# Kernel optimization log

Hardware: AMD Instinct MI355X
Metric: run time of the kernel (lower is better)

The kernel has to match this reference:

```python
import jax, jax.numpy as jnp
import numpy as np

N = 50000
E = 800000
F_IN = 256
HEADS = 4
C = 64
NEG_SLOPE = 0.2


def setup_inputs() -> dict:
    key = jax.random.key(0)
    ks = jax.random.split(key, 7)
    x = jax.random.normal(ks[0], (N, F_IN), dtype=jnp.float32)
    edge_index = jax.random.randint(ks[1], (2, E), 0, N, dtype=jnp.int64)
    # Glorot-ish scaling for weights
    W = jax.random.normal(ks[2], (F_IN, HEADS * C), dtype=jnp.float32) / np.sqrt(F_IN)
    att_src = jax.random.normal(ks[3], (HEADS, C), dtype=jnp.float32) / np.sqrt(C)
    att_dst = jax.random.normal(ks[4], (HEADS, C), dtype=jnp.float32) / np.sqrt(C)
    bias = jnp.zeros((HEADS * C,), dtype=jnp.float32)
    prelu_a = jnp.full((1,), 0.25, dtype=jnp.float32)  # PReLU default init
    return {"x": x, "edge_index": edge_index, "W": W, "att_src": att_src,
            "att_dst": att_dst, "bias": bias, "prelu_a": prelu_a}


def _gat_forward(x, edge_index, W, att_src, att_dst, bias, prelu_a):
    n = x.shape[0]
    # add self loops (PyG GATConv default)
    loops = jnp.arange(n, dtype=edge_index.dtype)
    src = jnp.concatenate([edge_index[0], loops])  # message source j
    dst = jnp.concatenate([edge_index[1], loops])  # message target i

    h = (x @ W).reshape(n, HEADS, C)                    # [N,H,C]
    a_src = jnp.einsum('nhc,hc->nh', h, att_src)        # [N,H]
    a_dst = jnp.einsum('nhc,hc->nh', h, att_dst)        # [N,H]

    e = a_src[src] + a_dst[dst]                         # [Etot,H]
    e = jnp.where(e >= 0, e, NEG_SLOPE * e)             # LeakyReLU(0.2)

    # numerically stable softmax over edges grouped by destination node
    m = jax.ops.segment_max(e, dst, num_segments=n)     # [N,H]
    alpha = jnp.exp(e - m[dst])
    denom = jax.ops.segment_sum(alpha, dst, num_segments=n)
    alpha = alpha / (denom[dst] + 1e-16)                # [Etot,H]

    msg = alpha[:, :, None] * h[src]                    # [Etot,H,C]
    out = jax.ops.segment_sum(msg, dst, num_segments=n) # [N,H,C]
    out = out.reshape(n, HEADS * C) + bias
    # PReLU with single shared parameter
    return jnp.where(out >= 0, out, prelu_a * out)


def reference(x, edge_index, W, att_src, att_dst, bias, prelu_a):
    return _gat_forward(x, edge_index, W, att_src, att_dst, bias, prelu_a)
```

## Files before the change

### kernel.cpp

```cpp
#include <hip/hip_runtime.h>
#include <stdint.h>


using u16 = unsigned short;
typedef float f32x4 __attribute__((ext_vector_type(4)));
typedef __bf16 bf16x8 __attribute__((ext_vector_type(8)));
typedef u16 u16x8 __attribute__((ext_vector_type(8)));

#define NEG 0.2f
#define APAD 264
#define NBLK1 256

__device__ __forceinline__ float bf2f(u16 u) {
    union { uint32_t i; float f; } v; v.i = ((uint32_t)u) << 16; return v.f;
}
__device__ __forceinline__ u16 f2bf(float f) {
    union { float f; uint32_t i; } v; v.f = f;
    uint32_t r = v.i + 0x7FFFu + ((v.i >> 16) & 1u);
    return (u16)(r >> 16);
}
__device__ __forceinline__ void split2(float f, u16& h, u16& l) {
    union { float f; uint32_t i; } v; v.f = f;
    h = (u16)(v.i >> 16);
    float r = f - bf2f(h);
    union { float f; uint32_t i; } w; w.f = r;
    l = (u16)(w.i >> 16);
}
__device__ __forceinline__ float wexp(float e) {
    e = e >= 0.f ? e : NEG * e;
    return __expf(e);
}

__global__ __launch_bounds__(256) void prep_kernel(
    const float* __restrict__ W, u16* __restrict__ Wfh, u16* __restrict__ Wfl,
    const int* __restrict__ edst, int* __restrict__ cnt1,
    int E, int Nn, int chunk)
{
    __shared__ int h1[256];
    const int tid = threadIdx.x, cb = blockIdx.x;
    h1[tid] = 0;
    __syncthreads();
    const int e0 = cb * chunk;
    const int e1 = (e0 + chunk < E) ? e0 + chunk : E;
    for (int e = e0 + tid; e < e1; e += 256) {
        int i = edst[e];
        i = ((unsigned)i < (unsigned)Nn) ? i : 0;
        atomicAdd(&h1[i >> 8], 1);
    }
    __syncthreads();
    cnt1[cb * 256 + tid] = h1[tid];

    if (cb < 32) {
        const int f = cb * 4 + (tid >> 6);
        const int l = tid & 63;
        const int kg = f >> 4, nb = f & 15;
        const int n = nb * 16 + (l & 15);
        const int kb = kg * 32 + (l >> 4) * 8;
        u16x8 hv, lv;
#pragma unroll
        for (int j = 0; j < 8; j++) {
            u16 th, tl;
            split2(W[(size_t)(kb + j) * 256 + n], th, tl);
            hv[j] = th;
            lv[j] = tl;
        }
        *(u16x8*)(Wfh + ((size_t)f * 64 + l) * 8) = hv;
        *(u16x8*)(Wfl + ((size_t)f * 64 + l) * 8) = lv;
    }
}

__global__ __launch_bounds__(256, 2) void mix_kernel(
    const float* __restrict__ X, const u16* __restrict__ Wfh,
    const u16* __restrict__ Wfl, const float* __restrict__ attS,
    const float* __restrict__ attD, u16* __restrict__ H,
    float* __restrict__ a_src, float* __restrict__ a_dst,
    const int* __restrict__ esrc, const int* __restrict__ edst,
    const int* __restrict__ cnt1, uint32_t* __restrict__ part,
    int E, int Nn, int chunk)
{
    __shared__ u16 Ah[64 * APAD];
    __shared__ u16 Al[64 * APAD];
    __shared__ int cur[256];
    __shared__ int wsum[4];
    const int tid = threadIdx.x;
    const int ln = tid & 63, wv = tid >> 6;

    if (blockIdx.x < NBLK1) {
        const int cb = blockIdx.x;
        int pre = 0, tot = 0;
        for (int c = 0; c < NBLK1; c++) {
            const int v = cnt1[c * 256 + tid];
            tot += v;
            pre += (c < cb) ? v : 0;
        }
        int s = tot;
#pragma unroll
        for (int o = 1; o < 64; o <<= 1) {
            int u = __shfl_up(s, o, 64);
            if (ln >= o) s += u;
        }
        if (ln == 63) wsum[wv] = s;
        __syncthreads();
        int wpre = 0;
#pragma unroll
        for (int w2 = 0; w2 < 4; w2++) wpre += (w2 < wv) ? wsum[w2] : 0;
        cur[tid] = (wpre + s - tot) + pre;
        __syncthreads();
        const int e0 = cb * chunk;
        const int e1 = (e0 + chunk < E) ? e0 + chunk : E;
        for (int e = e0 + tid; e < e1; e += 256) {
            int i = edst[e];
            i = ((unsigned)i < (unsigned)Nn) ? i : 0;
            int j = esrc[e];
            j = ((unsigned)j < (unsigned)Nn) ? j : 0;
            const int pos = atomicAdd(&cur[i >> 8], 1);
            part[pos] = (uint32_t)j | ((uint32_t)(i & 255) << 16);
        }
        return;
    }

    const int m0 = (blockIdx.x - NBLK1) * 64;
    const int wave = tid >> 6, lane = tid & 63;
    const int quad = lane >> 4, lr = lane & 15;

#pragma unroll
    for (int i = 0; i < 16; i++) {
        const int f = i * 256 + tid;
        const int row = f >> 6;
        const int c4 = (f & 63) * 4;
        int grow = m0 + row;
        if (grow >= Nn) grow = Nn - 1;
        const float4 v = *(const float4*)(X + (size_t)grow * 256 + c4);
        u16 h0, l0, h1, l1, h2, l2, h3, l3;
        split2(v.x, h0, l0); split2(v.y, h1, l1);
        split2(v.z, h2, l2); split2(v.w, h3, l3);
        uint2 hp, lp;
        hp.x = (uint32_t)h0 | ((uint32_t)h1 << 16);
        hp.y = (uint32_t)h2 | ((uint32_t)h3 << 16);
        lp.x = (uint32_t)l0 | ((uint32_t)l1 << 16);
        lp.y = (uint32_t)l2 | ((uint32_t)l3 << 16);
        *(uint2*)(Ah + row * APAD + c4) = hp;
        *(uint2*)(Al + row * APAD + c4) = lp;
    }
    __syncthreads();

    f32x4 acc[4][4] = {};
    bf16x8 bh[2][4], bl[2][4];

#pragma unroll
    for (int ni = 0; ni < 4; ni++) {
        const size_t o = ((size_t)(wave * 4 + ni) * 64 + lane) * 8;
        bh[0][ni] = *(const bf16x8*)(Wfh + o);
        bl[0][ni] = *(const bf16x8*)(Wfl + o);
    }

#pragma unroll
    for (int kg = 0; kg < 8; kg++) {
        const int st = kg & 1, ns = st ^ 1;
        if (kg < 7) {
#pragma unroll
            for (int ni = 0; ni < 4; ni++) {
                const size_t o = ((size_t)((kg + 1) * 16 + wave * 4 + ni) * 64 + lane) * 8;
                bh[ns][ni] = *(const bf16x8*)(Wfh + o);
                bl[ns][ni] = *(const bf16x8*)(Wfl + o);
            }
        }
        bf16x8 ah[4], al[4];
#pragma unroll
        for (int mi = 0; mi < 4; mi++) {
            const int o = (mi * 16 + lr) * APAD + kg * 32 + quad * 8;
            ah[mi] = *(const bf16x8*)(Ah + o);
            al[mi] = *(const bf16x8*)(Al + o);
        }
#pragma unroll
        for (int ni = 0; ni < 4; ni++)
#pragma unroll
            for (int mi = 0; mi < 4; mi++) {
                acc[mi][ni] = __builtin_amdgcn_mfma_f32_16x16x32_bf16(
                    ah[mi], bh[st][ni], acc[mi][ni], 0, 0, 0);
                acc[mi][ni] = __builtin_amdgcn_mfma_f32_16x16x32_bf16(
                    ah[mi], bl[st][ni], acc[mi][ni], 0, 0, 0);
                acc[mi][ni] = __builtin_amdgcn_mfma_f32_16x16x32_bf16(
                    al[mi], bh[st][ni], acc[mi][ni], 0, 0, 0);
            }
    }

    {
        float asv[4], adv[4];
#pragma unroll
        for (int ni = 0; ni < 4; ni++) {
            asv[ni] = attS[wave * 64 + ni * 16 + lr];
            adv[ni] = attD[wave * 64 + ni * 16 + lr];
        }
#pragma unroll
        for (int mi = 0; mi < 4; mi++)
#pragma unroll
            for (int r = 0; r < 4; r++) {
                float ps = 0.f, pd = 0.f;
#pragma unroll
                for (int ni = 0; ni < 4; ni++) {
                    ps += acc[mi][ni][r] * asv[ni];
                    pd += acc[mi][ni][r] * adv[ni];
                }
#pragma unroll
                for (int off = 8; off >= 1; off >>= 1) {
                    ps += __shfl_xor(ps, off, 16);
                    pd += __shfl_xor(pd, off, 16);
                }
                if (lr == 0) {
                    const int row = m0 + mi * 16 + quad * 4 + r;
                    if (row < Nn) {
                        a_src[row * 4 + wave] = ps;
                        a_dst[row * 4 + wave] = pd;
                    }
                }
            }
    }

    __syncthreads();
    const int n0 = wave * 64;
#pragma unroll
    for (int mi = 0; mi < 4; mi++)
#pragma unroll
        for (int ni = 0; ni < 4; ni++) {
            const int col = n0 + ni * 16 + lr;
#pragma unroll
            for (int r = 0; r < 4; r++)
                Ah[(mi * 16 + quad * 4 + r) * APAD + col] = f2bf(acc[mi][ni][r]);
        }
    __syncthreads();
#pragma unroll
    for (int swp = 0; swp < 8; swp++) {
        const int idx = swp * 256 + tid;
        const int row = idx >> 5;
        const int c16 = idx & 31;
        const int grow = m0 + row;
        if (grow < Nn)
            *(u16x8*)(H + (size_t)grow * 256 + c16 * 8) =
                *(const u16x8*)(Ah + row * APAD + c16 * 8);
    }
}

__global__ __launch_bounds__(256) void p2_kernel(
    const uint32_t* __restrict__ part, const int* __restrict__ cnt1,
    int* __restrict__ deg, int* __restrict__ offs, int* __restrict__ csr_src,
    int E, int Nn, int nb1)
{
    __shared__ int lds[256];
    __shared__ int wsum[4];
    __shared__ int sbd[2];
    const int b = blockIdx.x, tid = threadIdx.x;
    const int ln = tid & 63, wv = tid >> 6;

    int tot = 0;
    for (int c = 0; c < NBLK1; c++) tot += cnt1[c * 256 + tid];
    int s = tot;
#pragma unroll
    for (int o = 1; o < 64; o <<= 1) {
        int u = __shfl_up(s, o, 64);
        if (ln >= o) s += u;
    }
    if (ln == 63) wsum[wv] = s;
    __syncthreads();
    int wpre = 0;
#pragma unroll
    for (int w2 = 0; w2 < 4; w2++) wpre += (w2 < wv) ? wsum[w2] : 0;
    if (tid == b) { sbd[0] = wpre + s - tot; sbd[1] = wpre + s; }
    __syncthreads();
    const int bstart = sbd[0], bend = sbd[1];

    lds[tid] = 0;
    __syncthreads();
    for (int e = bstart + tid; e < bend; e += 256)
        atomicAdd(&lds[part[e] >> 16], 1);
    __syncthreads();
    const int cnt = lds[tid];
    int s2 = cnt;
#pragma unroll
    for (int o = 1; o < 64; o <<= 1) {
        int u = __shfl_up(s2, o, 64);
        if (ln >= o) s2 += u;
    }
    if (ln == 63) wsum[wv] = s2;
    __syncthreads();
    int wpre2 = 0;
#pragma unroll
    for (int w2 = 0; w2 < 4; w2++) wpre2 += (w2 < wv) ? wsum[w2] : 0;
    const int ex = bstart + wpre2 + s2 - cnt;
    const int node = (b << 8) + tid;
    if (node < Nn) { deg[node] = cnt; offs[node] = ex; }
    __syncthreads();
    lds[tid] = ex;
    __syncthreads();
    for (int e = bstart + tid; e < bend; e += 256) {
        const uint32_t pr = part[e];
        const int pos = atomicAdd(&lds[pr >> 16], 1);
        csr_src[pos] = (int)(pr & 0xFFFFu);
    }
}

__global__ __launch_bounds__(256) void gather_kernel(
    const u16* __restrict__ H, const int* __restrict__ offs,
    const int* __restrict__ deg, const int* __restrict__ csr_src,
    const float* __restrict__ a_src, const float* __restrict__ a_dst,
    const float* __restrict__ bias, const float* __restrict__ prelu,
    float* __restrict__ out, int Nn)
{
    const int wave = threadIdx.x >> 6, lane = threadIdx.x & 63;
    const int g = blockIdx.x >> 3, s = blockIdx.x & 7;
    const int hp = s >> 2;
    const int node = ((g << 2) + (s & 3)) * 4 + wave;
    if (node >= Nn) return;
    const int hh = lane >> 5;
    const int head = (hp << 1) + hh;
    const int sub = lane & 31;
    const int ch = (head << 6) + sub * 2;

    const float adv = a_dst[node * 4 + head];
    const float ws = wexp(a_src[node * 4 + head] + adv);
    float acc0, acc1, sumw = 0.f;
    {
        const uint32_t hv = *(const uint32_t*)(H + (size_t)node * 256 + ch);
        acc0 = ws * bf2f((u16)hv);
        acc1 = ws * bf2f((u16)(hv >> 16));
    }
    const int d = deg[node];
    const int* __restrict__ cp = csr_src + offs[node];

    for (int k = 0; k < d; k += 32) {
        const int q = d - k;
        const int es = (sub < q) ? sub : q - 1;
        const int jj = cp[k + es];
        float ww = wexp(a_src[jj * 4 + head] + adv);
        ww = (sub < q) ? ww : 0.f;
        sumw += ww;
        const int nh = (q > 16) ? 2 : 1;
        for (int half = 0; half < nh; half++) {
            const int hb = half << 4;
            uint32_t hv[16];
#pragma unroll
            for (int t = 0; t < 16; t++) {
                const int jt = __shfl(jj, hb + t, 32);
                hv[t] = *(const uint32_t*)(H + ((size_t)jt << 8) + ch);
            }
#pragma unroll
            for (int t = 0; t < 16; t++) {
                const float w = __shfl(ww, hb + t, 32);
                acc0 += w * bf2f((u16)hv[t]);
                acc1 += w * bf2f((u16)(hv[t] >> 16));
            }
        }
    }
#pragma unroll
    for (int off = 16; off >= 1; off >>= 1)
        sumw += __shfl_xor(sumw, off, 32);

    const float inv = 1.f / (ws + sumw + 1e-16f);
    const float pa = prelu[0];
    float o0 = acc0 * inv + bias[ch];
    float o1 = acc1 * inv + bias[ch + 1];
    o0 = o0 >= 0.f ? o0 : pa * o0;
    o1 = o1 >= 0.f ? o1 : pa * o1;
    float2 ov; ov.x = o0; ov.y = o1;
    *(float2*)(out + (size_t)node * 256 + ch) = ov;
}

extern "C" void kernel_launch(void* const* d_in, const int* in_sizes, int n_in,
                              void* d_out, int out_size, void* d_ws, size_t ws_size,
                              hipStream_t stream)
{
    const float* X    = (const float*)d_in[0];
    const int*   EI   = (const int*)d_in[1];
    const float* W    = (const float*)d_in[2];
    const float* attS = (const float*)d_in[3];
    const float* attD = (const float*)d_in[4];
    const float* bias = (const float*)d_in[5];
    const float* pa   = (const float*)d_in[6];

    const int Nn = in_sizes[0] / 256;
    const int E  = in_sizes[1] / 2;
    const int* esrc = EI;
    const int* edst = EI + E;

    const int nb1   = (Nn + 255) >> 8;
    const int chunk = (E + NBLK1 - 1) / NBLK1;

    char* p = (char*)d_ws;
    u16*      H       = (u16*)p;      p += (size_t)Nn * 256 * 2;
    float*    a_src   = (float*)p;    p += (size_t)Nn * 4 * 4;
    float*    a_dst   = (float*)p;    p += (size_t)Nn * 4 * 4;
    u16*      Wfh     = (u16*)p;      p += 256 * 256 * 2;
    u16*      Wfl     = (u16*)p;      p += 256 * 256 * 2;
    int*      deg     = (int*)p;      p += (size_t)Nn * 4;
    int*      offs    = (int*)p;      p += (size_t)Nn * 4;
    int*      cnt1    = (int*)p;      p += (size_t)NBLK1 * 256 * 4;
    uint32_t* part    = (uint32_t*)p; p += (size_t)E * 4;
    int*      csr_src = (int*)p;      p += ((size_t)E + 16) * 4;

    prep_kernel<<<NBLK1, 256, 0, stream>>>(W, Wfh, Wfl, edst, cnt1,
                                           E, Nn, chunk);
    const int gemmBlocks = (Nn + 63) / 64;
    mix_kernel<<<NBLK1 + gemmBlocks, 256, 0, stream>>>(
        X, Wfh, Wfl, attS, attD, H, a_src, a_dst,
        esrc, edst, cnt1, part, E, Nn, chunk);
    p2_kernel<<<nb1, 256, 0, stream>>>(part, cnt1, deg, offs, csr_src,
                                       E, Nn, nb1);
    const int gblocks = ((Nn + 15) / 16) * 8;
    gather_kernel<<<gblocks, 256, 0, stream>>>(H, offs, deg, csr_src,
                                               a_src, a_dst, bias, pa,
                                               (float*)d_out, Nn);
}
```

Before: 237.2 us.

## Split gather wave over one head with two edge-parallel halves

The gather kernel now gives each wave a single (node, head) pair instead of two heads. The two 32-lane halves of the wave take alternating edges from a 64-edge chunk, and their partial accumulators are combined with a cross-half shuffle at the end. This doubles the grid size and is meant to raise memory-level parallelism and occupancy for the irregular H row gathers, which matters because average degree is low (about 17). The cost is twice the a_dst/a_src/deg/offs reads per node, an extra reduction step, and only half the lanes doing the final store.

```diff
diff --git a/kernel.cpp b/kernel.cpp
--- a/kernel.cpp
+++ b/kernel.cpp
@@ -308,61 +308,63 @@
 {
     const int wave = threadIdx.x >> 6, lane = threadIdx.x & 63;
     const int g = blockIdx.x >> 3, s = blockIdx.x & 7;
-    const int hp = s >> 2;
-    const int node = ((g << 2) + (s & 3)) * 4 + wave;
+    const int head = s >> 1;
+    const int node = ((g << 1) + (s & 1)) * 4 + wave;
     if (node >= Nn) return;
-    const int hh = lane >> 5;
-    const int head = (hp << 1) + hh;
-    const int sub = lane & 31;
-    const int ch = (head << 6) + sub * 2;
+    const int p = lane >> 5;
+    const int cp2 = lane & 31;
+    const int ch = (head << 6) + cp2 * 2;
 
     const float adv = a_dst[node * 4 + head];
     const float ws = wexp(a_src[node * 4 + head] + adv);
-    float acc0, acc1, sumw = 0.f;
-    {
-        const uint32_t hv = *(const uint32_t*)(H + (size_t)node * 256 + ch);
-        acc0 = ws * bf2f((u16)hv);
-        acc1 = ws * bf2f((u16)(hv >> 16));
-    }
+    const uint32_t hself = *(const uint32_t*)(H + (size_t)node * 256 + ch);
+    float acc0 = 0.f, acc1 = 0.f, sumw = 0.f;
+
     const int d = deg[node];
     const int* __restrict__ cp = csr_src + offs[node];
 
-    for (int k = 0; k < d; k += 32) {
+    for (int k = 0; k < d; k += 64) {
         const int q = d - k;
-        const int es = (sub < q) ? sub : q - 1;
+        const int es = (lane < q) ? lane : q - 1;
         const int jj = cp[k + es];
         float ww = wexp(a_src[jj * 4 + head] + adv);
-        ww = (sub < q) ? ww : 0.f;
+        ww = (lane < q) ? ww : 0.f;
         sumw += ww;
-        const int nh = (q > 16) ? 2 : 1;
-        for (int half = 0; half < nh; half++) {
-            const int hb = half << 4;
-            uint32_t hv[16];
-#pragma unroll
-            for (int t = 0; t < 16; t++) {
-                const int jt = __shfl(jj, hb + t, 32);
-                hv[t] = *(const uint32_t*)(H + ((size_t)jt << 8) + ch);
+#pragma unroll
+        for (int g0 = 0; g0 < 64; g0 += 16) {
+            if (g0 >= q) break;
+            uint32_t hv[8];
+#pragma unroll
+            for (int i = 0; i < 8; i++) {
+                const int r = g0 + 2 * i + p;
+                const int jt = __shfl(jj, r, 64);
+                hv[i] = *(const uint32_t*)(H + ((size_t)jt << 8) + ch);
             }
 #pragma unroll
-            for (int t = 0; t < 16; t++) {
-                const float w = __shfl(ww, hb + t, 32);
-                acc0 += w * bf2f((u16)hv[t]);
-                acc1 += w * bf2f((u16)(hv[t] >> 16));
+            for (int i = 0; i < 8; i++) {
+                const int r = g0 + 2 * i + p;
+                const float w = __shfl(ww, r, 64);
+                acc0 += w * bf2f((u16)hv[i]);
+                acc1 += w * bf2f((u16)(hv[i] >> 16));
             }
         }
     }
-#pragma unroll
-    for (int off = 16; off >= 1; off >>= 1)
-        sumw += __shfl_xor(sumw, off, 32);
-
-    const float inv = 1.f / (ws + sumw + 1e-16f);
-    const float pa = prelu[0];
-    float o0 = acc0 * inv + bias[ch];
-    float o1 = acc1 * inv + bias[ch + 1];
-    o0 = o0 >= 0.f ? o0 : pa * o0;
-    o1 = o1 >= 0.f ? o1 : pa * o1;
-    float2 ov; ov.x = o0; ov.y = o1;
-    *(float2*)(out + (size_t)node * 256 + ch) = ov;
+    acc0 += __shfl_xor(acc0, 32, 64);
+    acc1 += __shfl_xor(acc1, 32, 64);
+#pragma unroll
+    for (int off = 32; off >= 1; off >>= 1)
+        sumw += __shfl_xor(sumw, off, 64);
+
+    if (p == 0) {
+        const float inv = 1.f / (ws + sumw + 1e-16f);
+        const float pa = prelu[0];
+        float o0 = (acc0 + ws * bf2f((u16)hself)) * inv + bias[ch];
+        float o1 = (acc1 + ws * bf2f((u16)(hself >> 16))) * inv + bias[ch + 1];
+        o0 = o0 >= 0.f ? o0 : pa * o0;
+        o1 = o1 >= 0.f ? o1 : pa * o1;
+        float2 ov; ov.x = o0; ov.y = o1;
+        *(float2*)(out + (size_t)node * 256 + ch) = ov;
+    }
 }
 
 extern "C" void kernel_launch(void* const* d_in, const int* in_sizes, int n_in,
@@ -405,7 +407,7 @@
         esrc, edst, cnt1, part, E, Nn, chunk);
     p2_kernel<<<nb1, 256, 0, stream>>>(part, cnt1, deg, offs, csr_src,
                                        E, Nn, nb1);
-    const int gblocks = ((Nn + 15) / 16) * 8;
+    const int gblocks = ((Nn + 7) / 8) * 8;
     gather_kernel<<<gblocks, 256, 0, stream>>>(H, offs, deg, csr_src,
                                                a_src, a_dst, bias, pa,
                                                (float*)d_out, Nn);
```

Result: slower. 255.2 us (+7.6%).
